# Kernel tuning notes

Measured on AMD Instinct MI355X. Metric: run time of the kernel, lower is better.

## Reference

```python
import jax, jax.numpy as jnp
import numpy as np

N = 4000; T_GRU = 32; T_TREE = 16; F = 256; HS = 128; H = 3 * HS; CC = 512; E = 64000; D4 = 4 * HS


def _gru_last(x, wi, wh, bi, bh):
    # x: [N, T, F]; torch GRU gate order r, z, n. Returns last hidden [N, H].
    xp = jnp.einsum('ntf,gf->ntg', x, wi) + bi  # [N, T, 3H]
    h0 = jnp.zeros((x.shape[0], wh.shape[1]), x.dtype)
    def step(h, xt):
        gh = h @ wh.T + bh
        ir, iz, inn = jnp.split(xt, 3, axis=1)
        hr, hz, hn = jnp.split(gh, 3, axis=1)
        r = jax.nn.sigmoid(ir + hr)
        z = jax.nn.sigmoid(iz + hz)
        n = jnp.tanh(inn + r * hn)
        return (1.0 - z) * n + z * h, None
    hT, _ = jax.lax.scan(step, h0, jnp.swapaxes(xp, 0, 1))
    return hT


def _tree_root(x, ioux_w, ioux_b, iouh_w, iouh_b, fx_w, fx_b, fh_w, fh_b):
    # Chain-structured TreeLSTM (each node has one child); x: [N, T, F], leaf-to-root.
    xi = jnp.einsum('ntf,gf->ntg', x, ioux_w) + ioux_b  # [N, T, 3M]
    xf = jnp.einsum('ntf,mf->ntm', x, fx_w) + fx_b      # [N, T, M]
    M = fh_w.shape[0]
    z0 = jnp.zeros((x.shape[0], M), x.dtype)
    def step(carry, xs):
        c, h = carry
        xi_t, xf_t = xs
        iou = xi_t + h @ iouh_w.T + iouh_b
        i, o, u = jnp.split(iou, 3, axis=1)
        f = jax.nn.sigmoid(xf_t + h @ fh_w.T + fh_b)
        c = jax.nn.sigmoid(i) * jnp.tanh(u) + f * c
        h = jax.nn.sigmoid(o) * jnp.tanh(c)
        return (c, h), None
    (c, h), _ = jax.lax.scan(step, (z0, z0), (jnp.swapaxes(xi, 0, 1), jnp.swapaxes(xf, 0, 1)))
    return h


def _gcn(x, w, b, row, col):
    # PyG GCNConv: self-loops + symmetric normalization.
    n = x.shape[0]
    xw = x @ w.T
    loops = jnp.arange(n, dtype=row.dtype)
    r = jnp.concatenate([row, loops])
    c = jnp.concatenate([col, loops])
    deg = jax.ops.segment_sum(jnp.ones(r.shape, x.dtype), c, num_segments=n)
    dinv = jnp.where(deg > 0, jax.lax.rsqrt(jnp.maximum(deg, 1e-12)), 0.0)
    norm = (dinv[r] * dinv[c])[:, None]
    return jax.ops.segment_sum(xw[r] * norm, c, num_segments=n) + b


def setup_inputs() -> dict:
    key = jax.random.key(0)
    ks = jax.random.split(key, 48)
    s = 0.05
    p = lambda i, sh: jax.random.normal(ks[i], sh, jnp.float32) * s
    return {
        'feat1': p(0, (N, T_GRU, F)),
        'feat2': p(1, (N, T_TREE, F)),
        'feat3': p(2, (N, T_TREE, F)),
        'feat4': p(3, (N, CC)),
        'edge_index': jax.random.randint(ks[4], (2, E), 0, N),
        'gru_wi': p(5, (3 * H, F)), 'gru_wh': p(6, (3 * H, H)),
        'gru_bi': p(7, (3 * H,)), 'gru_bh': p(8, (3 * H,)),
        't1_ioux_w': p(9, (3 * H, F)), 't1_ioux_b': p(10, (3 * H,)),
        't1_iouh_w': p(11, (3 * H, H)), 't1_iouh_b': p(12, (3 * H,)),
        't1_fx_w': p(13, (H, F)), 't1_fx_b': p(14, (H,)),
        't1_fh_w': p(15, (H, H)), 't1_fh_b': p(16, (H,)),
        't2_ioux_w': p(17, (3 * H, F)), 't2_ioux_b': p(18, (3 * H,)),
        't2_iouh_w': p(19, (3 * H, H)), 't2_iouh_b': p(20, (3 * H,)),
        't2_fx_w': p(21, (H, F)), 't2_fx_b': p(22, (H,)),
        't2_fh_w': p(23, (H, H)), 't2_fh_b': p(24, (H,)),
        'r1_w': p(25, (HS, H)), 'r1_b': p(26, (HS,)),
        'r2_w': p(27, (HS, H)), 'r2_b': p(28, (HS,)),
        'r3_w': p(29, (HS, H)), 'r3_b': p(30, (HS,)),
        'r4_w': p(31, (HS, CC)), 'r4_b': p(32, (HS,)),
        'gcn0_w': p(33, (D4, D4)), 'gcn0_b': p(34, (D4,)),
        'gcn1_w': p(35, (D4, D4)), 'gcn1_b': p(36, (D4,)),
        'r7_w': p(37, (2, D4)), 'r7_b': p(38, (2,)),
    }


def reference(feat1, feat2, feat3, feat4, edge_index,
              gru_wi, gru_wh, gru_bi, gru_bh,
              t1_ioux_w, t1_ioux_b, t1_iouh_w, t1_iouh_b, t1_fx_w, t1_fx_b, t1_fh_w, t1_fh_b,
              t2_ioux_w, t2_ioux_b, t2_iouh_w, t2_iouh_b, t2_fx_w, t2_fx_b, t2_fh_w, t2_fh_b,
              r1_w, r1_b, r2_w, r2_b, r3_w, r3_b, r4_w, r4_b,
              gcn0_w, gcn0_b, gcn1_w, gcn1_b, r7_w, r7_b):
    v1 = _gru_last(feat1, gru_wi, gru_wh, gru_bi, gru_bh)            # [N, H]
    v2 = _tree_root(feat2, t1_ioux_w, t1_ioux_b, t1_iouh_w, t1_iouh_b, t1_fx_w, t1_fx_b, t1_fh_w, t1_fh_b)
    v3 = _tree_root(feat3, t2_ioux_w, t2_ioux_b, t2_iouh_w, t2_iouh_b, t2_fx_w, t2_fx_b, t2_fh_w, t2_fh_b)
    f1 = v1 @ r1_w.T + r1_b
    f2 = v2 @ r2_w.T + r2_b
    f3 = v3 @ r3_w.T + r3_b
    f4 = feat4 @ r4_w.T + r4_b
    m = jnp.concatenate([f1, f2, f3, f4], axis=1)                    # [N, 4*HS]
    row, col = edge_index[0], edge_index[1]
    m = jax.nn.relu(_gcn(m, gcn0_w, gcn0_b, row, col))
    m = _gcn(m, gcn1_w, gcn1_b, row, col)
    m = jax.nn.softmax(m @ r7_w.T + r7_b, axis=1)                    # [N, 2]
    return m.T                                                       # [2, N]
```

## Files before the change

kernel.cpp:

```cpp
#include <hip/hip_runtime.h>
#include <hip/hip_bf16.h>
#include <math.h>

#define NN 4000
#define TG 32
#define TT 16
#define FF 256
#define HH 384
#define GCOLS 1536
#define KCAT 640
#define EE 64000
#define D4 512

typedef __attribute__((ext_vector_type(8))) short short8;
typedef __attribute__((ext_vector_type(4))) float float4v;

static __device__ __forceinline__ float fsig(float x)  { return 1.0f / (1.0f + __expf(-x)); }
static __device__ __forceinline__ float ftanh(float x) { return 2.0f / (1.0f + __expf(-2.0f*x)) - 1.0f; }

static __device__ __forceinline__ void async_copy16(const void* g, void* l) {
    __builtin_amdgcn_global_load_lds(
        (const __attribute__((address_space(1))) unsigned int*)g,
        (__attribute__((address_space(3))) unsigned int*)l, 16, 0, 0);
}

__global__ __launch_bounds__(256) void prep_w_kernel(
    const float* __restrict__ gwi, const float* __restrict__ gwh,
    const float* __restrict__ gbi, const float* __restrict__ gbh,
    const float* __restrict__ x1w, const float* __restrict__ x1b,
    const float* __restrict__ h1w, const float* __restrict__ h1b,
    const float* __restrict__ fx1w, const float* __restrict__ fx1b,
    const float* __restrict__ fh1w, const float* __restrict__ fh1b,
    const float* __restrict__ x2w, const float* __restrict__ x2b,
    const float* __restrict__ h2w, const float* __restrict__ h2b,
    const float* __restrict__ fx2w, const float* __restrict__ fx2b,
    const float* __restrict__ fh2w, const float* __restrict__ fh2b,
    __hip_bfloat16* __restrict__ Wp, float* __restrict__ bp)
{
    int z = blockIdx.z;
    int idx = blockIdx.x * 256 + threadIdx.x;
    int c = idx / KCAT, k = idx - c * KCAT;
    int bx = c >> 7, wc = (c >> 6) & 1, g = (c >> 4) & 3, rl = c & 15;
    int j = bx*32 + wc*16 + rl;
    float v = 0.0f, bv = 0.0f;
    if (z == 0) {
        if (g <= 1) {
            int row = g*HH + j;
            v = (k < FF) ? gwi[row*FF + k] : gwh[row*HH + (k-FF)];
            bv = gbi[row] + gbh[row];
        } else if (g == 2) {
            int row = 2*HH + j;
            v = (k < FF) ? gwi[row*FF + k] : 0.0f;
            bv = gbi[row];
        } else {
            int row = 2*HH + j;
            v = (k < FF) ? 0.0f : gwh[row*HH + (k-FF)];
            bv = gbh[row];
        }
    } else {
        const float* xw  = (z==1)? x1w  : x2w;   const float* xb  = (z==1)? x1b  : x2b;
        const float* hw  = (z==1)? h1w  : h2w;   const float* hb_ = (z==1)? h1b  : h2b;
        const float* fxw = (z==1)? fx1w : fx2w;  const float* fxb = (z==1)? fx1b : fx2b;
        const float* fhw = (z==1)? fh1w : fh2w;  const float* fhb = (z==1)? fh1b : fh2b;
        if (g < 3) {
            int row = g*HH + j;
            v = (k < FF) ? xw[row*FF + k] : hw[row*HH + (k-FF)];
            bv = xb[row] + hb_[row];
        } else {
            v = (k < FF) ? fxw[j*FF + k] : fhw[j*HH + (k-FF)];
            bv = fxb[j] + fhb[j];
        }
    }
    Wp[(size_t)z*GCOLS*KCAT + idx] = __float2bfloat16(v);
    if (k == 0) bp[z*GCOLS + c] = bv;
}

__global__ __launch_bounds__(256) void f2b_kernel(const float* __restrict__ s,
                                                  __hip_bfloat16* __restrict__ d, int n)
{
    int i = blockIdx.x*256 + threadIdx.x;
    if (i < n) d[i] = __float2bfloat16(s[i]);
}

__global__ __launch_bounds__(256) void tpose_kernel(const float* __restrict__ f1,
    const float* __restrict__ f2, const float* __restrict__ f3,
    __hip_bfloat16* __restrict__ xg, __hip_bfloat16* __restrict__ xt)
{
    int zz = blockIdx.z;
    int gid = blockIdx.x*256 + threadIdx.x;
    int T = (zz == 0) ? TG : TT;
    int rows = NN * T;
    int rowid = gid >> 6;
    if (rowid >= rows) return;
    int f = (gid & 63) * 4;
    int n = rowid / T, t = rowid - n*T;
    const float* src = (zz==0)? f1 : (zz==1)? f2 : f3;
    float4 v = *(const float4*)(src + (size_t)rowid*FF + f);
    __hip_bfloat16* dst = (zz==0)? xg : (xt + (size_t)(zz-1)*TT*NN*FF);
    __hip_bfloat16 b4[4] = {__float2bfloat16(v.x), __float2bfloat16(v.y),
                            __float2bfloat16(v.z), __float2bfloat16(v.w)};
    *(ushort4*)(dst + ((size_t)t*NN + n)*FF + f) = *(const ushort4*)b4;
}

#define BM 128
#define BN 128
#define BKK 32

template<int MODE>
__global__ __launch_bounds__(256) void gemm_k(
    const __hip_bfloat16* __restrict__ Xb, size_t zX, int ldx, int k1,
    const __hip_bfloat16* __restrict__ Hin, size_t zH,
    const __hip_bfloat16* __restrict__ Wb, size_t zW, int K,
    const float* __restrict__ bp, size_t zB, int hasBias,
    const float* __restrict__ Sin, size_t zS,
    float* __restrict__ Sout, size_t zSo,
    __hip_bfloat16* __restrict__ Hout, size_t zHo,
    int ldC, int M)
{
    const int z = blockIdx.z;
    const __hip_bfloat16* X  = Xb + zX*z;
    const __hip_bfloat16* Hi = (MODE != 0) ? (Hin + zH*z) : nullptr;
    const __hip_bfloat16* W  = Wb + zW*z;

    __shared__ __align__(16) __hip_bfloat16 As[BM][BKK];
    __shared__ __align__(16) __hip_bfloat16 Bs[BN][BKK];

    const int tid  = threadIdx.x;
    const int lane = tid & 63;
    const int w    = tid >> 6;
    const int wr = w >> 1, wc = w & 1;
    const int rowBase = blockIdx.y * BM;
    const int colBase = blockIdx.x * BN;
    const int sRow = tid >> 2;
    const int sK   = (tid & 3) * 8;

    float4v acc[4][4];
    #pragma unroll
    for (int i = 0; i < 4; ++i)
        #pragma unroll
        for (int j = 0; j < 4; ++j)
            acc[i][j] = (float4v){0.f, 0.f, 0.f, 0.f};

    const int rl = lane & 15;
    const int kl = (lane >> 4) * 8;

    for (int kt = 0; kt < K; kt += BKK) {
        const int kk = kt + sK;
        #pragma unroll
        for (int i = 0; i < 2; ++i) {
            int r = i*64 + sRow;
            int gr = rowBase + r; if (gr > M-1) gr = M-1;
            const __hip_bfloat16* src;
            if (MODE == 0 || kk < k1) src = X  + (size_t)gr*ldx + kk;
            else                      src = Hi + (size_t)gr*HH + (kk - k1);
            async_copy16(src, &As[r][sK]);
        }
        #pragma unroll
        for (int i = 0; i < 2; ++i) {
            int r = i*64 + sRow;
            async_copy16(W + (size_t)(colBase + r)*K + kk, &Bs[r][sK]);
        }
        __syncthreads();

        short8 af[4], bfr[4];
        #pragma unroll
        for (int mi = 0; mi < 4; ++mi)
            af[mi] = *(const short8*)&As[wr*64 + mi*16 + rl][kl];
        #pragma unroll
        for (int ni = 0; ni < 4; ++ni)
            bfr[ni] = *(const short8*)&Bs[wc*64 + ni*16 + rl][kl];
        #pragma unroll
        for (int mi = 0; mi < 4; ++mi)
            #pragma unroll
            for (int ni = 0; ni < 4; ++ni)
                acc[mi][ni] = __builtin_amdgcn_mfma_f32_16x16x32_bf16(af[mi], bfr[ni], acc[mi][ni], 0, 0, 0);
        __syncthreads();
    }

    const int rq = (lane >> 4) * 4;

    if (MODE == 0) {
        float* C = Sout + zSo*z;
        __hip_bfloat16* C16 = Hout ? (Hout + zHo*z) : nullptr;
        #pragma unroll
        for (int mi = 0; mi < 4; ++mi) {
            #pragma unroll
            for (int q = 0; q < 4; ++q) {
                int row = rowBase + wr*64 + mi*16 + rq + q;
                if (row >= M) continue;
                #pragma unroll
                for (int ni = 0; ni < 4; ++ni) {
                    int col = colBase + wc*64 + ni*16 + rl;
                    float v = acc[mi][ni][q];
                    if (hasBias) v += bp[zB*z + col];
                    C[(size_t)row*ldC + col] = v;
                    if (C16) C16[(size_t)row*ldC + col] = __float2bfloat16(v);
                }
            }
        }
    } else {
        const int j = (colBase >> 2) + wc*16 + rl;
        const int cb = colBase + wc*64 + rl;
        float b0 = bp[zB*z + cb + 0];
        float b1 = bp[zB*z + cb + 16];
        float b2 = bp[zB*z + cb + 32];
        float b3 = bp[zB*z + cb + 48];
        const float* Si = Sin + zS*z;
        float* So = Sout + zSo*z;
        __hip_bfloat16* Ho = Hout + zHo*z;
        #pragma unroll
        for (int mi = 0; mi < 4; ++mi) {
            #pragma unroll
            for (int q = 0; q < 4; ++q) {
                int row = rowBase + wr*64 + mi*16 + rq + q;
                if (row >= M) continue;
                float g0 = acc[mi][0][q] + b0;
                float g1 = acc[mi][1][q] + b1;
                float g2 = acc[mi][2][q] + b2;
                float g3 = acc[mi][3][q] + b3;
                size_t off = (size_t)row*HH + j;
                if (MODE == 1) {
                    float r  = fsig(g0), zz = fsig(g1);
                    float n  = ftanh(g2 + r*g3);
                    float hp = Si[off];
                    float hn = (1.0f - zz)*n + zz*hp;
                    So[off] = hn;
                    Ho[off] = __float2bfloat16(hn);
                } else {
                    float cp = Si[off];
                    float cn = fsig(g0)*ftanh(g2) + fsig(g3)*cp;
                    So[off] = cn;
                    float hn = fsig(g1)*ftanh(cn);
                    Ho[off] = __float2bfloat16(hn);
                }
            }
        }
    }
}

__global__ __launch_bounds__(256) void count_kernel(const int* __restrict__ col, int* __restrict__ degi)
{
    int e = blockIdx.x*256 + threadIdx.x;
    if (e < EE) atomicAdd(&degi[col[e]], 1);
}

__global__ __launch_bounds__(1024) void scan_kernel(const int* __restrict__ degi,
    int* __restrict__ start, int* __restrict__ cursor, float* __restrict__ dinv)
{
    __shared__ int s[1024];
    int t = threadIdx.x;
    int v[4]; int sum = 0;
    #pragma unroll
    for (int i = 0; i < 4; ++i) {
        int idx = t*4 + i;
        v[i] = (idx < NN) ? degi[idx] : 0;
        sum += v[i];
    }
    s[t] = sum;
    __syncthreads();
    for (int d = 1; d < 1024; d <<= 1) {
        int x = (t >= d) ? s[t-d] : 0;
        __syncthreads();
        s[t] += x;
        __syncthreads();
    }
    int base = s[t] - sum;
    int run = 0;
    #pragma unroll
    for (int i = 0; i < 4; ++i) {
        int idx = t*4 + i;
        if (idx < NN) {
            int st = base + run;
            start[idx] = st;
            cursor[idx] = st;
            dinv[idx] = rsqrtf((float)v[i] + 1.0f);
        }
        run += v[i];
    }
    if (t == 1023) start[NN] = s[1023];
}

__global__ __launch_bounds__(256) void fill_kernel(const int* __restrict__ row,
    const int* __restrict__ col, int* __restrict__ cursor, int* __restrict__ esrc)
{
    int e = blockIdx.x*256 + threadIdx.x;
    if (e < EE) {
        int c = col[e];
        int pos = atomicAdd(&cursor[c], 1);
        esrc[pos] = row[e];
    }
}

__global__ __launch_bounds__(256) void gather_kernel(const float* __restrict__ xw,
    const int* __restrict__ esrc, const int* __restrict__ start,
    const float* __restrict__ dinv, const float* __restrict__ bias,
    float* __restrict__ mout, __hip_bfloat16* __restrict__ mout16, int relu)
{
    int wv = threadIdx.x >> 6, lane = threadIdx.x & 63;
    int n = blockIdx.x*4 + wv;
    if (n >= NN) return;
    float a[8] = {0.f,0.f,0.f,0.f,0.f,0.f,0.f,0.f};
    int s0 = start[n], s1 = start[n+1];
    float dn = dinv[n];
    for (int e = s0; e < s1; ++e) {
        int r = esrc[e];
        float nrm = dinv[r]*dn;
        const float4 v0 = *(const float4*)(xw + (size_t)r*D4 + lane*8);
        const float4 v1 = *(const float4*)(xw + (size_t)r*D4 + lane*8 + 4);
        a[0] += v0.x*nrm; a[1] += v0.y*nrm; a[2] += v0.z*nrm; a[3] += v0.w*nrm;
        a[4] += v1.x*nrm; a[5] += v1.y*nrm; a[6] += v1.z*nrm; a[7] += v1.w*nrm;
    }
    const float4 u0 = *(const float4*)(xw + (size_t)n*D4 + lane*8);
    const float4 u1 = *(const float4*)(xw + (size_t)n*D4 + lane*8 + 4);
    float dd = dn*dn;
    float su[8] = {u0.x,u0.y,u0.z,u0.w,u1.x,u1.y,u1.z,u1.w};
    #pragma unroll
    for (int i = 0; i < 8; ++i) {
        float vv = a[i] + su[i]*dd + bias[lane*8 + i];
        if (relu) vv = fmaxf(vv, 0.0f);
        mout[(size_t)n*D4 + lane*8 + i] = vv;
        if (mout16) mout16[(size_t)n*D4 + lane*8 + i] = __float2bfloat16(vv);
    }
}

__global__ __launch_bounds__(256) void final_kernel(const float* __restrict__ m,
    const float* __restrict__ w, const float* __restrict__ b, float* __restrict__ out)
{
    int wave = threadIdx.x >> 6;
    int lane = threadIdx.x & 63;
    int n = blockIdx.x*4 + wave;
    const float* row = m + (size_t)n*D4 + lane*8;
    float4 v0 = *(const float4*)(row);
    float4 v1 = *(const float4*)(row + 4);
    const float* w0 = w + lane*8;
    const float* w1 = w + D4 + lane*8;
    float4 u0 = *(const float4*)(w0); float4 u1 = *(const float4*)(w0 + 4);
    float4 t0 = *(const float4*)(w1); float4 t1 = *(const float4*)(w1 + 4);
    float a = v0.x*u0.x + v0.y*u0.y + v0.z*u0.z + v0.w*u0.w
            + v1.x*u1.x + v1.y*u1.y + v1.z*u1.z + v1.w*u1.w;
    float bb = v0.x*t0.x + v0.y*t0.y + v0.z*t0.z + v0.w*t0.w
             + v1.x*t1.x + v1.y*t1.y + v1.z*t1.z + v1.w*t1.w;
    #pragma unroll
    for (int s = 32; s; s >>= 1) { a += __shfl_xor(a, s); bb += __shfl_xor(bb, s); }
    if (lane == 0) {
        float l0 = a + b[0], l1 = bb + b[1];
        float mx = fmaxf(l0, l1);
        float e0 = expf(l0 - mx), e1 = expf(l1 - mx);
        float s = e0 + e1;
        out[n]      = e0 / s;
        out[NN + n] = e1 / s;
    }
}

extern "C" void kernel_launch(void* const* d_in, const int* in_sizes, int n_in,
                              void* d_out, int out_size, void* d_ws, size_t ws_size,
                              hipStream_t stream)
{
    const float* feat1 = (const float*)d_in[0];
    const float* feat2 = (const float*)d_in[1];
    const float* feat3 = (const float*)d_in[2];
    const float* feat4 = (const float*)d_in[3];
    const int*   eidx  = (const int*)d_in[4];
    const float* r1w = (const float*)d_in[25]; const float* r1b = (const float*)d_in[26];
    const float* r2w = (const float*)d_in[27]; const float* r2b = (const float*)d_in[28];
    const float* r3w = (const float*)d_in[29]; const float* r3b = (const float*)d_in[30];
    const float* r4w = (const float*)d_in[31]; const float* r4b = (const float*)d_in[32];
    const float* g0w = (const float*)d_in[33]; const float* g0b = (const float*)d_in[34];
    const float* g1w = (const float*)d_in[35]; const float* g1b = (const float*)d_in[36];
    const float* r7w = (const float*)d_in[37]; const float* r7b = (const float*)d_in[38];

    float* ws = (float*)d_ws;
    size_t o = 0;
    auto alloc = [&](size_t nfl) { float* p = ws + o; o += (nfl + 3) & ~(size_t)3; return p; };

    float* hf0 = alloc((size_t)NN*HH);
    float* cf0 = alloc((size_t)2*NN*HH);
    __hip_bfloat16* hb0 = (__hip_bfloat16*)alloc((size_t)3*NN*HH/2);
    size_t zeroFloats = o;
    float* hf1 = alloc((size_t)NN*HH);
    float* cf1 = alloc((size_t)2*NN*HH);
    __hip_bfloat16* hb1 = (__hip_bfloat16*)alloc((size_t)3*NN*HH/2);
    __hip_bfloat16* xg  = (__hip_bfloat16*)alloc((size_t)TG*NN*FF/2);
    __hip_bfloat16* xt  = (__hip_bfloat16*)alloc((size_t)2*TT*NN*FF/2);
    __hip_bfloat16* Wp  = (__hip_bfloat16*)alloc((size_t)3*GCOLS*KCAT/2);
    float* bp   = alloc(3*GCOLS);
    float* mbuf = alloc((size_t)NN*D4);
    float* xwb  = alloc((size_t)NN*D4);
    float* dinv = alloc(NN);
    __hip_bfloat16* mbf16 = (__hip_bfloat16*)alloc((size_t)NN*D4/2);
    __hip_bfloat16* f4b   = (__hip_bfloat16*)alloc((size_t)NN*D4/2);
    __hip_bfloat16* rw123 = (__hip_bfloat16*)alloc((size_t)3*128*HH/2);
    float* rb123 = alloc(3*128);
    __hip_bfloat16* r4w16 = (__hip_bfloat16*)alloc((size_t)128*D4/2);
    __hip_bfloat16* g0w16 = (__hip_bfloat16*)alloc((size_t)D4*D4/2);
    __hip_bfloat16* g1w16 = (__hip_bfloat16*)alloc((size_t)D4*D4/2);
    int* degi   = (int*)alloc(NN);
    int* start  = (int*)alloc(NN + 4);
    int* cursor = (int*)alloc(NN);
    int* esrc   = (int*)alloc(EE);

    float* hfp[2] = {hf0, hf1};
    float* cfp[2] = {cf0, cf1};
    __hip_bfloat16* hbp[2] = {hb0, hb1};

    hipMemsetAsync(hf0, 0, zeroFloats*sizeof(float), stream);
    hipMemsetAsync(degi, 0, NN*sizeof(int), stream);

    prep_w_kernel<<<dim3(3840,1,3),256,0,stream>>>(
        (const float*)d_in[5],(const float*)d_in[6],(const float*)d_in[7],(const float*)d_in[8],
        (const float*)d_in[9],(const float*)d_in[10],(const float*)d_in[11],(const float*)d_in[12],
        (const float*)d_in[13],(const float*)d_in[14],(const float*)d_in[15],(const float*)d_in[16],
        (const float*)d_in[17],(const float*)d_in[18],(const float*)d_in[19],(const float*)d_in[20],
        (const float*)d_in[21],(const float*)d_in[22],(const float*)d_in[23],(const float*)d_in[24],
        Wp, bp);

    tpose_kernel<<<dim3(32000,1,3),256,0,stream>>>(feat1, feat2, feat3, xg, xt);
    f2b_kernel<<<8000,256,0,stream>>>(feat4, f4b, NN*D4);
    f2b_kernel<<<192,256,0,stream>>>(r1w, rw123, 128*HH);
    f2b_kernel<<<192,256,0,stream>>>(r2w, rw123 + 128*HH, 128*HH);
    f2b_kernel<<<192,256,0,stream>>>(r3w, rw123 + 2*128*HH, 128*HH);
    f2b_kernel<<<256,256,0,stream>>>(r4w, r4w16, 128*D4);
    f2b_kernel<<<1024,256,0,stream>>>(g0w, g0w16, D4*D4);
    f2b_kernel<<<1024,256,0,stream>>>(g1w, g1w16, D4*D4);
    hipMemcpyAsync(rb123,       r1b, 128*sizeof(float), hipMemcpyDeviceToDevice, stream);
    hipMemcpyAsync(rb123 + 128, r2b, 128*sizeof(float), hipMemcpyDeviceToDevice, stream);
    hipMemcpyAsync(rb123 + 256, r3b, 128*sizeof(float), hipMemcpyDeviceToDevice, stream);

    count_kernel<<<250,256,0,stream>>>(eidx + EE, degi);
    scan_kernel<<<1,1024,0,stream>>>(degi, start, cursor, dinv);
    fill_kernel<<<250,256,0,stream>>>(eidx, eidx + EE, cursor, esrc);

    for (int t = 0; t < TG; ++t) {
        int p = t & 1, q = p ^ 1;
        gemm_k<1><<<dim3(GCOLS/BN, 32, 1),256,0,stream>>>(
            xg + (size_t)t*NN*FF, 0, FF, FF,
            hbp[p], 0,
            Wp, 0, KCAT,
            bp, 0, 1,
            hfp[p], 0,
            hfp[q], 0,
            hbp[q], 0,
            HH, NN);
    }
    for (int t = 0; t < TT; ++t) {
        int p = t & 1, q = p ^ 1;
        gemm_k<2><<<dim3(GCOLS/BN, 32, 2),256,0,stream>>>(
            xt + (size_t)t*NN*FF, (size_t)TT*NN*FF, FF, FF,
            hbp[p] + (size_t)NN*HH, (size_t)NN*HH,
            Wp + (size_t)GCOLS*KCAT, (size_t)GCOLS*KCAT, KCAT,
            bp + GCOLS, GCOLS, 1,
            cfp[p], (size_t)NN*HH,
            cfp[q], (size_t)NN*HH,
            hbp[q] + (size_t)NN*HH, (size_t)NN*HH,
            HH, NN);
    }

    gemm_k<0><<<dim3(1,32,3),256,0,stream>>>(
        hbp[0], (size_t)NN*HH, HH, HH, nullptr, 0,
        rw123, (size_t)128*HH, HH,
        rb123, 128, 1,
        nullptr, 0, mbuf, 128,
        mbf16, 128, D4, NN);
    gemm_k<0><<<dim3(1,32,1),256,0,stream>>>(
        f4b, 0, D4, D4, nullptr, 0,
        r4w16, 0, D4,
        r4b, 0, 1,
        nullptr, 0, mbuf + 384, 0,
        mbf16 + 384, 0, D4, NN);

    gemm_k<0><<<dim3(4,32,1),256,0,stream>>>(
        mbf16, 0, D4, D4, nullptr, 0,
        g0w16, 0, D4,
        nullptr, 0, 0,
        nullptr, 0, xwb, 0,
        nullptr, 0, D4, NN);
    gather_kernel<<<1000,256,0,stream>>>(xwb, esrc, start, dinv, g0b, mbuf, mbf16, 1);

    gemm_k<0><<<dim3(4,32,1),256,0,stream>>>(
        mbf16, 0, D4, D4, nullptr, 0,
        g1w16, 0, D4,
        nullptr, 0, 0,
        nullptr, 0, xwb, 0,
        nullptr, 0, D4, NN);
    gather_kernel<<<1000,256,0,stream>>>(xwb, esrc, start, dinv, g1b, mbuf, nullptr, 0);

    final_kernel<<<1000,256,0,stream>>>(mbuf, r7w, r7b, (float*)d_out);
}
```

Measured before the change: 1.705 ms.

## Hoist input projections out of recurrences into batched chunked GEMMs

Precomputes the input-to-gate projections (x·Wx + bias) for chunks of timesteps with one large GEMM per chunk, writing bf16 results time-major. The per-step kernel then only multiplies h by Wh (K=384 instead of 640) using 64-row tiles for more blocks. The transpose kernel is removed and the permutation is folded into the A-row indexing, and the conversion kernels are vectorised. This adds a large bf16 intermediate buffer and rounds the x projection to bf16, which may shift accuracy slightly.

```diff
diff --git a/kernel.cpp b/kernel.cpp
--- a/kernel.cpp
+++ b/kernel.cpp
@@ -17,6 +17,12 @@
 
 static __device__ __forceinline__ float fsig(float x)  { return 1.0f / (1.0f + __expf(-x)); }
 static __device__ __forceinline__ float ftanh(float x) { return 2.0f / (1.0f + __expf(-2.0f*x)) - 1.0f; }
+static __device__ __forceinline__ float bf2f(unsigned short u) {
+    union { unsigned int i; float f; } x; x.i = ((unsigned int)u) << 16; return x.f;
+}
+static __device__ __forceinline__ unsigned short f2bf(float f) {
+    __hip_bfloat16 h = __float2bfloat16(f); return *reinterpret_cast<unsigned short*>(&h);
+}
 
 static __device__ __forceinline__ void async_copy16(const void* g, void* l) {
     __builtin_amdgcn_global_load_lds(
@@ -35,7 +41,8 @@
     const float* __restrict__ h2w, const float* __restrict__ h2b,
     const float* __restrict__ fx2w, const float* __restrict__ fx2b,
     const float* __restrict__ fh2w, const float* __restrict__ fh2b,
-    __hip_bfloat16* __restrict__ Wp, float* __restrict__ bp)
+    __hip_bfloat16* __restrict__ Wx, __hip_bfloat16* __restrict__ Wh,
+    float* __restrict__ bp)
 {
     int z = blockIdx.z;
     int idx = blockIdx.x * 256 + threadIdx.x;
@@ -71,56 +78,37 @@
             bv = fxb[j] + fhb[j];
         }
     }
-    Wp[(size_t)z*GCOLS*KCAT + idx] = __float2bfloat16(v);
+    if (k < FF) Wx[(size_t)z*GCOLS*FF + (size_t)c*FF + k] = __float2bfloat16(v);
+    else        Wh[(size_t)z*GCOLS*HH + (size_t)c*HH + (k-FF)] = __float2bfloat16(v);
     if (k == 0) bp[z*GCOLS + c] = bv;
 }
 
-__global__ __launch_bounds__(256) void f2b_kernel(const float* __restrict__ s,
-                                                  __hip_bfloat16* __restrict__ d, int n)
+__global__ __launch_bounds__(256) void f2b4_kernel(const float* __restrict__ s,
+                                                   __hip_bfloat16* __restrict__ d, int n4)
 {
     int i = blockIdx.x*256 + threadIdx.x;
-    if (i < n) d[i] = __float2bfloat16(s[i]);
-}
-
-__global__ __launch_bounds__(256) void tpose_kernel(const float* __restrict__ f1,
-    const float* __restrict__ f2, const float* __restrict__ f3,
-    __hip_bfloat16* __restrict__ xg, __hip_bfloat16* __restrict__ xt)
-{
-    int zz = blockIdx.z;
-    int gid = blockIdx.x*256 + threadIdx.x;
-    int T = (zz == 0) ? TG : TT;
-    int rows = NN * T;
-    int rowid = gid >> 6;
-    if (rowid >= rows) return;
-    int f = (gid & 63) * 4;
-    int n = rowid / T, t = rowid - n*T;
-    const float* src = (zz==0)? f1 : (zz==1)? f2 : f3;
-    float4 v = *(const float4*)(src + (size_t)rowid*FF + f);
-    __hip_bfloat16* dst = (zz==0)? xg : (xt + (size_t)(zz-1)*TT*NN*FF);
-    __hip_bfloat16 b4[4] = {__float2bfloat16(v.x), __float2bfloat16(v.y),
-                            __float2bfloat16(v.z), __float2bfloat16(v.w)};
-    *(ushort4*)(dst + ((size_t)t*NN + n)*FF + f) = *(const ushort4*)b4;
+    if (i >= n4) return;
+    float4 v = ((const float4*)s)[i];
+    ushort4 u = { f2bf(v.x), f2bf(v.y), f2bf(v.z), f2bf(v.w) };
+    ((ushort4*)d)[i] = u;
 }
 
 #define BM 128
 #define BN 128
 #define BKK 32
 
-template<int MODE>
-__global__ __launch_bounds__(256) void gemm_k(
-    const __hip_bfloat16* __restrict__ Xb, size_t zX, int ldx, int k1,
-    const __hip_bfloat16* __restrict__ Hin, size_t zH,
+__global__ __launch_bounds__(256) void gemm0_k(
+    const __hip_bfloat16* __restrict__ Ab, size_t zA, int lda,
     const __hip_bfloat16* __restrict__ Wb, size_t zW, int K,
-    const float* __restrict__ bp, size_t zB, int hasBias,
-    const float* __restrict__ Sin, size_t zS,
-    float* __restrict__ Sout, size_t zSo,
-    __hip_bfloat16* __restrict__ Hout, size_t zHo,
-    int ldC, int M)
+    const float* __restrict__ bias, size_t zB,
+    float* __restrict__ C, size_t zC,
+    __hip_bfloat16* __restrict__ C16, size_t zC16,
+    int ldC, int M,
+    int perm, int tcShift, int logT, int t0)
 {
     const int z = blockIdx.z;
-    const __hip_bfloat16* X  = Xb + zX*z;
-    const __hip_bfloat16* Hi = (MODE != 0) ? (Hin + zH*z) : nullptr;
-    const __hip_bfloat16* W  = Wb + zW*z;
+    const __hip_bfloat16* A = Ab + zA*z;
+    const __hip_bfloat16* W = Wb + zW*z;
 
     __shared__ __align__(16) __hip_bfloat16 As[BM][BKK];
     __shared__ __align__(16) __hip_bfloat16 Bs[BN][BKK];
@@ -133,6 +121,7 @@
     const int colBase = blockIdx.x * BN;
     const int sRow = tid >> 2;
     const int sK   = (tid & 3) * 8;
+    const int tcMask = (1 << tcShift) - 1;
 
     float4v acc[4][4];
     #pragma unroll
@@ -148,12 +137,10 @@
         const int kk = kt + sK;
         #pragma unroll
         for (int i = 0; i < 2; ++i) {
-            int r = i*64 + sRow;
-            int gr = rowBase + r; if (gr > M-1) gr = M-1;
-            const __hip_bfloat16* src;
-            if (MODE == 0 || kk < k1) src = X  + (size_t)gr*ldx + kk;
-            else                      src = Hi + (size_t)gr*HH + (kk - k1);
-            async_copy16(src, &As[r][sK]);
+            int gr = rowBase + i*64 + sRow;
+            if (gr > M-1) gr = M-1;
+            int arow = perm ? (((gr >> tcShift) << logT) + t0 + (gr & tcMask)) : gr;
+            async_copy16(A + (size_t)arow*lda + kk, &As[i*64 + sRow][sK]);
         }
         #pragma unroll
         for (int i = 0; i < 2; ++i) {
@@ -179,9 +166,9 @@
 
     const int rq = (lane >> 4) * 4;
 
-    if (MODE == 0) {
-        float* C = Sout + zSo*z;
-        __hip_bfloat16* C16 = Hout ? (Hout + zHo*z) : nullptr;
+    if (!perm) {
+        float* Cz = C + zC*z;
+        __hip_bfloat16* C16z = C16 ? (C16 + zC16*z) : nullptr;
         #pragma unroll
         for (int mi = 0; mi < 4; ++mi) {
             #pragma unroll
@@ -192,47 +179,133 @@
                 for (int ni = 0; ni < 4; ++ni) {
                     int col = colBase + wc*64 + ni*16 + rl;
                     float v = acc[mi][ni][q];
-                    if (hasBias) v += bp[zB*z + col];
-                    C[(size_t)row*ldC + col] = v;
-                    if (C16) C16[(size_t)row*ldC + col] = __float2bfloat16(v);
+                    if (bias) v += bias[zB*z + col];
+                    Cz[(size_t)row*ldC + col] = v;
+                    if (C16z) C16z[(size_t)row*ldC + col] = __float2bfloat16(v);
                 }
             }
         }
     } else {
-        const int j = (colBase >> 2) + wc*16 + rl;
+        __hip_bfloat16* C16z = C16 + zC16*z;
         const int cb = colBase + wc*64 + rl;
-        float b0 = bp[zB*z + cb + 0];
-        float b1 = bp[zB*z + cb + 16];
-        float b2 = bp[zB*z + cb + 32];
-        float b3 = bp[zB*z + cb + 48];
-        const float* Si = Sin + zS*z;
-        float* So = Sout + zSo*z;
-        __hip_bfloat16* Ho = Hout + zHo*z;
+        float b0 = bias[zB*z + cb + 0];
+        float b1 = bias[zB*z + cb + 16];
+        float b2 = bias[zB*z + cb + 32];
+        float b3 = bias[zB*z + cb + 48];
         #pragma unroll
         for (int mi = 0; mi < 4; ++mi) {
             #pragma unroll
             for (int q = 0; q < 4; ++q) {
                 int row = rowBase + wr*64 + mi*16 + rq + q;
                 if (row >= M) continue;
-                float g0 = acc[mi][0][q] + b0;
-                float g1 = acc[mi][1][q] + b1;
-                float g2 = acc[mi][2][q] + b2;
-                float g3 = acc[mi][3][q] + b3;
-                size_t off = (size_t)row*HH + j;
-                if (MODE == 1) {
-                    float r  = fsig(g0), zz = fsig(g1);
-                    float n  = ftanh(g2 + r*g3);
-                    float hp = Si[off];
-                    float hn = (1.0f - zz)*n + zz*hp;
-                    So[off] = hn;
-                    Ho[off] = __float2bfloat16(hn);
-                } else {
-                    float cp = Si[off];
-                    float cn = fsig(g0)*ftanh(g2) + fsig(g3)*cp;
-                    So[off] = cn;
-                    float hn = fsig(g1)*ftanh(cn);
-                    Ho[off] = __float2bfloat16(hn);
-                }
+                int outRow = (row & tcMask)*NN + (row >> tcShift);
+                ushort4 uv = { f2bf(acc[mi][0][q] + b0), f2bf(acc[mi][1][q] + b1),
+                               f2bf(acc[mi][2][q] + b2), f2bf(acc[mi][3][q] + b3) };
+                *(ushort4*)(C16z + (size_t)outRow*ldC + colBase + wc*64 + rl*4) = uv;
+            }
+        }
+    }
+}
+
+#define SBM 64
+
+template<int MODE>
+__global__ __launch_bounds__(256) void step_k(
+    const __hip_bfloat16* __restrict__ Hin, size_t zH,
+    const __hip_bfloat16* __restrict__ Whb, size_t zW,
+    const __hip_bfloat16* __restrict__ xp, size_t zXp,
+    const float* __restrict__ Sin, size_t zS,
+    float* __restrict__ Sout, size_t zSo,
+    __hip_bfloat16* __restrict__ Hout, size_t zHo)
+{
+    const int z = blockIdx.z;
+    const __hip_bfloat16* A   = Hin + zH*z;
+    const __hip_bfloat16* W   = Whb + zW*z;
+    const __hip_bfloat16* xpz = xp + zXp*z;
+    const float* Si = Sin + zS*z;
+    float* So = Sout + zSo*z;
+    __hip_bfloat16* Ho = Hout + zHo*z;
+
+    __shared__ __align__(16) __hip_bfloat16 As[SBM][BKK];
+    __shared__ __align__(16) __hip_bfloat16 Bs[BN][BKK];
+
+    const int tid  = threadIdx.x;
+    const int lane = tid & 63;
+    const int w    = tid >> 6;
+    const int wr = w >> 1, wc = w & 1;
+    const int rowBase = blockIdx.y * SBM;
+    const int colBase = blockIdx.x * BN;
+    const int sRow = tid >> 2;
+    const int sK   = (tid & 3) * 8;
+
+    float4v acc[2][4];
+    #pragma unroll
+    for (int i = 0; i < 2; ++i)
+        #pragma unroll
+        for (int j = 0; j < 4; ++j)
+            acc[i][j] = (float4v){0.f, 0.f, 0.f, 0.f};
+
+    const int rl = lane & 15;
+    const int kl = (lane >> 4) * 8;
+
+    for (int kt = 0; kt < HH; kt += BKK) {
+        const int kk = kt + sK;
+        {
+            int gr = rowBase + sRow;
+            if (gr > NN-1) gr = NN-1;
+            async_copy16(A + (size_t)gr*HH + kk, &As[sRow][sK]);
+        }
+        #pragma unroll
+        for (int i = 0; i < 2; ++i) {
+            int r = i*64 + sRow;
+            async_copy16(W + (size_t)(colBase + r)*HH + kk, &Bs[r][sK]);
+        }
+        __syncthreads();
+
+        short8 af[2], bfr[4];
+        #pragma unroll
+        for (int mi = 0; mi < 2; ++mi)
+            af[mi] = *(const short8*)&As[wr*32 + mi*16 + rl][kl];
+        #pragma unroll
+        for (int ni = 0; ni < 4; ++ni)
+            bfr[ni] = *(const short8*)&Bs[wc*64 + ni*16 + rl][kl];
+        #pragma unroll
+        for (int mi = 0; mi < 2; ++mi)
+            #pragma unroll
+            for (int ni = 0; ni < 4; ++ni)
+                acc[mi][ni] = __builtin_amdgcn_mfma_f32_16x16x32_bf16(af[mi], bfr[ni], acc[mi][ni], 0, 0, 0);
+        __syncthreads();
+    }
+
+    const int rq = (lane >> 4) * 4;
+    const int j  = (colBase >> 2) + wc*16 + rl;
+    const int xcol = colBase + wc*64 + rl*4;
+
+    #pragma unroll
+    for (int mi = 0; mi < 2; ++mi) {
+        #pragma unroll
+        for (int q = 0; q < 4; ++q) {
+            int row = rowBase + wr*32 + mi*16 + rq + q;
+            if (row >= NN) continue;
+            ushort4 xv = *(const ushort4*)(xpz + (size_t)row*GCOLS + xcol);
+            float g0 = acc[mi][0][q] + bf2f(xv.x);
+            float g1 = acc[mi][1][q] + bf2f(xv.y);
+            float g2 = acc[mi][2][q] + bf2f(xv.z);
+            float g3 = acc[mi][3][q] + bf2f(xv.w);
+            size_t off = (size_t)row*HH + j;
+            if (MODE == 1) {
+                float r  = fsig(g0), zz = fsig(g1);
+                float n  = ftanh(g2 + r*g3);
+                float hp = Si[off];
+                float hn = (1.0f - zz)*n + zz*hp;
+                So[off] = hn;
+                Ho[off] = __float2bfloat16(hn);
+            } else {
+                float cp = Si[off];
+                float cn = fsig(g0)*ftanh(g2) + fsig(g3)*cp;
+                So[off] = cn;
+                float hn = fsig(g1)*ftanh(cn);
+                Ho[off] = __float2bfloat16(hn);
             }
         }
     }
@@ -382,7 +455,9 @@
     __hip_bfloat16* hb1 = (__hip_bfloat16*)alloc((size_t)3*NN*HH/2);
     __hip_bfloat16* xg  = (__hip_bfloat16*)alloc((size_t)TG*NN*FF/2);
     __hip_bfloat16* xt  = (__hip_bfloat16*)alloc((size_t)2*TT*NN*FF/2);
-    __hip_bfloat16* Wp  = (__hip_bfloat16*)alloc((size_t)3*GCOLS*KCAT/2);
+    __hip_bfloat16* xpb = (__hip_bfloat16*)alloc((size_t)16*NN*GCOLS/2);
+    __hip_bfloat16* Wx  = (__hip_bfloat16*)alloc((size_t)3*GCOLS*FF/2);
+    __hip_bfloat16* Wh  = (__hip_bfloat16*)alloc((size_t)3*GCOLS*HH/2);
     float* bp   = alloc(3*GCOLS);
     float* mbuf = alloc((size_t)NN*D4);
     float* xwb  = alloc((size_t)NN*D4);
@@ -412,16 +487,18 @@
         (const float*)d_in[13],(const float*)d_in[14],(const float*)d_in[15],(const float*)d_in[16],
         (const float*)d_in[17],(const float*)d_in[18],(const float*)d_in[19],(const float*)d_in[20],
         (const float*)d_in[21],(const float*)d_in[22],(const float*)d_in[23],(const float*)d_in[24],
-        Wp, bp);
-
-    tpose_kernel<<<dim3(32000,1,3),256,0,stream>>>(feat1, feat2, feat3, xg, xt);
-    f2b_kernel<<<8000,256,0,stream>>>(feat4, f4b, NN*D4);
-    f2b_kernel<<<192,256,0,stream>>>(r1w, rw123, 128*HH);
-    f2b_kernel<<<192,256,0,stream>>>(r2w, rw123 + 128*HH, 128*HH);
-    f2b_kernel<<<192,256,0,stream>>>(r3w, rw123 + 2*128*HH, 128*HH);
-    f2b_kernel<<<256,256,0,stream>>>(r4w, r4w16, 128*D4);
-    f2b_kernel<<<1024,256,0,stream>>>(g0w, g0w16, D4*D4);
-    f2b_kernel<<<1024,256,0,stream>>>(g1w, g1w16, D4*D4);
+        Wx, Wh, bp);
+
+    f2b4_kernel<<<32000,256,0,stream>>>(feat1, xg, TG*NN*FF/4);
+    f2b4_kernel<<<16000,256,0,stream>>>(feat2, xt, TT*NN*FF/4);
+    f2b4_kernel<<<16000,256,0,stream>>>(feat3, xt + (size_t)TT*NN*FF, TT*NN*FF/4);
+    f2b4_kernel<<<2000,256,0,stream>>>(feat4, f4b, NN*D4/4);
+    f2b4_kernel<<<48,256,0,stream>>>(r1w, rw123, 128*HH/4);
+    f2b4_kernel<<<48,256,0,stream>>>(r2w, rw123 + 128*HH, 128*HH/4);
+    f2b4_kernel<<<48,256,0,stream>>>(r3w, rw123 + 2*128*HH, 128*HH/4);
+    f2b4_kernel<<<64,256,0,stream>>>(r4w, r4w16, 128*D4/4);
+    f2b4_kernel<<<256,256,0,stream>>>(g0w, g0w16, D4*D4/4);
+    f2b4_kernel<<<256,256,0,stream>>>(g1w, g1w16, D4*D4/4);
     hipMemcpyAsync(rb123,       r1b, 128*sizeof(float), hipMemcpyDeviceToDevice, stream);
     hipMemcpyAsync(rb123 + 128, r2b, 128*sizeof(float), hipMemcpyDeviceToDevice, stream);
     hipMemcpyAsync(rb123 + 256, r3b, 128*sizeof(float), hipMemcpyDeviceToDevice, stream);
@@ -430,58 +507,52 @@
     scan_kernel<<<1,1024,0,stream>>>(degi, start, cursor, dinv);
     fill_kernel<<<250,256,0,stream>>>(eidx, eidx + EE, cursor, esrc);
 
-    for (int t = 0; t < TG; ++t) {
-        int p = t & 1, q = p ^ 1;
-        gemm_k<1><<<dim3(GCOLS/BN, 32, 1),256,0,stream>>>(
-            xg + (size_t)t*NN*FF, 0, FF, FF,
-            hbp[p], 0,
-            Wp, 0, KCAT,
-            bp, 0, 1,
-            hfp[p], 0,
-            hfp[q], 0,
-            hbp[q], 0,
-            HH, NN);
-    }
-    for (int t = 0; t < TT; ++t) {
-        int p = t & 1, q = p ^ 1;
-        gemm_k<2><<<dim3(GCOLS/BN, 32, 2),256,0,stream>>>(
-            xt + (size_t)t*NN*FF, (size_t)TT*NN*FF, FF, FF,
-            hbp[p] + (size_t)NN*HH, (size_t)NN*HH,
-            Wp + (size_t)GCOLS*KCAT, (size_t)GCOLS*KCAT, KCAT,
-            bp + GCOLS, GCOLS, 1,
-            cfp[p], (size_t)NN*HH,
-            cfp[q], (size_t)NN*HH,
-            hbp[q] + (size_t)NN*HH, (size_t)NN*HH,
-            HH, NN);
-    }
-
-    gemm_k<0><<<dim3(1,32,3),256,0,stream>>>(
-        hbp[0], (size_t)NN*HH, HH, HH, nullptr, 0,
-        rw123, (size_t)128*HH, HH,
-        rb123, 128, 1,
-        nullptr, 0, mbuf, 128,
-        mbf16, 128, D4, NN);
-    gemm_k<0><<<dim3(1,32,1),256,0,stream>>>(
-        f4b, 0, D4, D4, nullptr, 0,
-        r4w16, 0, D4,
-        r4b, 0, 1,
-        nullptr, 0, mbuf + 384, 0,
-        mbf16 + 384, 0, D4, NN);
-
-    gemm_k<0><<<dim3(4,32,1),256,0,stream>>>(
-        mbf16, 0, D4, D4, nullptr, 0,
-        g0w16, 0, D4,
-        nullptr, 0, 0,
-        nullptr, 0, xwb, 0,
-        nullptr, 0, D4, NN);
+    for (int c = 0; c < 2; ++c) {
+        gemm0_k<<<dim3(GCOLS/BN, 500, 1),256,0,stream>>>(
+            xg, 0, FF, Wx, 0, FF, bp, 0,
+            nullptr, 0, xpb, 0, GCOLS, 16*NN,
+            1, 4, 5, c*16);
+        for (int tt = 0; tt < 16; ++tt) {
+            int t = c*16 + tt;
+            int p = t & 1, q = p ^ 1;
+            step_k<1><<<dim3(GCOLS/BN, 63, 1),256,0,stream>>>(
+                hbp[p], 0, Wh, 0,
+                xpb + (size_t)tt*NN*GCOLS, 0,
+                hfp[p], 0, hfp[q], 0, hbp[q], 0);
+        }
+    }
+    for (int c = 0; c < 2; ++c) {
+        gemm0_k<<<dim3(GCOLS/BN, 250, 2),256,0,stream>>>(
+            xt, (size_t)TT*NN*FF, FF, Wx + (size_t)GCOLS*FF, (size_t)GCOLS*FF, FF, bp + GCOLS, GCOLS,
+            nullptr, 0, xpb, (size_t)8*NN*GCOLS, GCOLS, 8*NN,
+            1, 3, 4, c*8);
+        for (int tt = 0; tt < 8; ++tt) {
+            int t = c*8 + tt;
+            int p = t & 1, q = p ^ 1;
+            step_k<2><<<dim3(GCOLS/BN, 63, 2),256,0,stream>>>(
+                hbp[p] + (size_t)NN*HH, (size_t)NN*HH,
+                Wh + (size_t)GCOLS*HH, (size_t)GCOLS*HH,
+                xpb + (size_t)tt*NN*GCOLS, (size_t)8*NN*GCOLS,
+                cfp[p], (size_t)NN*HH, cfp[q], (size_t)NN*HH,
+                hbp[q] + (size_t)NN*HH, (size_t)NN*HH);
+        }
+    }
+
+    gemm0_k<<<dim3(1,32,3),256,0,stream>>>(
+        hbp[0], (size_t)NN*HH, HH, rw123, (size_t)128*HH, HH, rb123, 128,
+        mbuf, 128, mbf16, 128, D4, NN, 0, 0, 0, 0);
+    gemm0_k<<<dim3(1,32,1),256,0,stream>>>(
+        f4b, 0, D4, r4w16, 0, D4, r4b, 0,
+        mbuf + 384, 0, mbf16 + 384, 0, D4, NN, 0, 0, 0, 0);
+
+    gemm0_k<<<dim3(4,32,1),256,0,stream>>>(
+        mbf16, 0, D4, g0w16, 0, D4, nullptr, 0,
+        xwb, 0, nullptr, 0, D4, NN, 0, 0, 0, 0);
     gather_kernel<<<1000,256,0,stream>>>(xwb, esrc, start, dinv, g0b, mbuf, mbf16, 1);
 
-    gemm_k<0><<<dim3(4,32,1),256,0,stream>>>(
-        mbf16, 0, D4, D4, nullptr, 0,
-        g1w16, 0, D4,
-        nullptr, 0, 0,
-        nullptr, 0, xwb, 0,
-        nullptr, 0, D4, NN);
+    gemm0_k<<<dim3(4,32,1),256,0,stream>>>(
+        mbf16, 0, D4, g1w16, 0, D4, nullptr, 0,
+        xwb, 0, nullptr, 0, D4, NN, 0, 0, 0, 0);
     gather_kernel<<<1000,256,0,stream>>>(xwb, esrc, start, dinv, g1b, mbuf, nullptr, 0);
 
     final_kernel<<<1000,256,0,stream>>>(mbuf, r7w, r7b, (float*)d_out);
```

Result: slower. 1.879 ms (+10.2%).
